# Kernel optimization log

Hardware: AMD Instinct MI355X
Metric: run time of the kernel (lower is better)

The kernel has to match this reference:

```python
import jax, jax.numpy as jnp
import numpy as np

# Dims: B batch, T snippets, DV visual feat (1024), DA audio feat (128),
# H hid_dim (128), DF ffn dim (512), KC classifier kernel (7)
B, T, DV, DA, H, DF, KC = 128, 256, 1024, 128, 128, 512, 7


def _xavier(key, shape, fan_in, fan_out):
    a = (6.0 / (fan_in + fan_out)) ** 0.5
    return jax.random.uniform(key, shape, jnp.float32, -a, a)


def setup_inputs() -> dict:
    key = jax.random.key(0)
    ks = jax.random.split(key, 9)
    return {
        "x": jax.random.normal(ks[0], (B, T, DV + DA), jnp.float32),
        # CrossAttention: q from audio (DA->H), k,v from visual (DV->H), out proj H->DV
        "Wq": _xavier(ks[1], (DA, H), DA, H), "bq": jnp.zeros((H,), jnp.float32),
        "Wk": _xavier(ks[2], (DV, H), DV, H), "bk": jnp.zeros((H,), jnp.float32),
        "Wv": _xavier(ks[3], (DV, H), DV, H), "bv": jnp.zeros((H,), jnp.float32),
        "Wo": _xavier(ks[4], (H, DV), H, DV), "bo": jnp.zeros((DV,), jnp.float32),
        # LayerNorm over modal_a=1024
        "ln_g": jnp.ones((DV,), jnp.float32), "ln_b": jnp.zeros((DV,), jnp.float32),
        # FFN: Conv1d(1024,512,1) -> GELU -> Conv1d(512,128,1) == two linears over channels
        "W1": _xavier(ks[5], (DV, DF), DV, DF), "b1": jnp.zeros((DF,), jnp.float32),
        "W2": _xavier(ks[6], (DF, H), DF, H), "b2": jnp.zeros((H,), jnp.float32),
        # Classifier: Conv1d(128, 1, kernel=7), OIH layout
        "Wc": _xavier(ks[7], (1, H, KC), H * KC, KC), "bc": jnp.zeros((1,), jnp.float32),
    }


def _distance_adj(t: int) -> jnp.ndarray:
    # adj[i, j] = exp(-|i - j| / e)  (DistanceAdj from the repo)
    idx = jnp.arange(t, dtype=jnp.float32)
    return jnp.exp(-jnp.abs(idx[:, None] - idx[None, :]) / jnp.float32(np.e))


def reference(x, Wq, bq, Wk, bk, Wv, bv, Wo, bo, ln_g, ln_b, W1, b1, W2, b2, Wc, bc):
    f_v = x[:, :, :DV]   # [B, T, 1024]
    f_a = x[:, :, DV:]   # [B, T, 128]
    adj = _distance_adj(T)  # [T, T], broadcast over batch

    # Cross attention: query from audio, key/value from visual, adjacency bias
    q = f_a @ Wq + bq                               # [B, T, H]
    k = f_v @ Wk + bk                               # [B, T, H]
    v = f_v @ Wv + bv                               # [B, T, H]
    scores = jnp.einsum('bqh,bkh->bqk', q, k) / jnp.sqrt(jnp.float32(H)) + adj
    attn = jax.nn.softmax(scores, axis=-1)
    ctx = jnp.einsum('bqk,bkh->bqh', attn, v)       # [B, T, H]
    ca_out = ctx @ Wo + bo                          # [B, T, 1024]

    # residual + LayerNorm(modal_a)
    h = f_v + ca_out
    mu = jnp.mean(h, axis=-1, keepdims=True)
    var = jnp.mean(jnp.square(h - mu), axis=-1, keepdims=True)
    h = (h - mu) * jax.lax.rsqrt(var + 1e-5) * ln_g + ln_b

    # conv1d(k=1) FFN: 1024 -> 512 -> GELU -> 128 (dropout = identity at eval)
    h = jax.nn.gelu(h @ W1 + b1, approximate=False) @ W2 + b2   # [B, T, 128]

    # causal left pad 6, then Conv1d(128 -> 1, kernel 7)
    hc = jnp.pad(jnp.transpose(h, (0, 2, 1)), ((0, 0), (0, 0), (KC - 1, 0)))  # [B, 128, T+6]
    logits = jax.lax.conv_general_dilated(
        hc, Wc, window_strides=(1,), padding='VALID',
        dimension_numbers=('NCH', 'OIH', 'NCH')) + bc[None, :, None]           # [B, 1, T]
    return jax.nn.sigmoid(logits[:, 0, :])                                      # [B, T]
```

## Files before the change

### kernel.cpp

```cpp
#include <hip/hip_runtime.h>
#include <hip/hip_bf16.h>
#include <math.h>

#define BB 128
#define TT 256
#define DV 1024
#define DA 128
#define HH 128
#define DF 512
#define KC 7
#define MM (BB*TT)

typedef __attribute__((ext_vector_type(8))) short    short8v;
typedef __attribute__((ext_vector_type(8))) _Float16 half8v;
typedef __attribute__((ext_vector_type(4))) float    float4v;

__device__ __forceinline__ float gelu_exact(float v) {
    return 0.5f * v * (1.0f + erff(v * 0.70710678118654752f));
}
__device__ __forceinline__ ushort f2h(float f) {
    _Float16 h = (_Float16)f;
    return __builtin_bit_cast(ushort, h);
}
__device__ __forceinline__ float h2f(ushort u) {
    _Float16 h = __builtin_bit_cast(_Float16, u);
    return (float)h;
}

__global__ __launch_bounds__(256) void wconv_kernel(const float* __restrict__ W,
                                                    ushort* __restrict__ Th,
                                                    int K, int N)
{
    __shared__ float sT[64][65];
    const int n0 = blockIdx.x * 64, k0 = blockIdx.y * 64;
    const int t = threadIdx.x;
    const int kk = t >> 4, n4 = (t & 15) * 4;
#pragma unroll
    for (int i = 0; i < 4; ++i) {
        float4 f = *(const float4*)(W + (size_t)(k0 + kk + i * 16) * N + n0 + n4);
        sT[kk + i * 16][n4 + 0] = f.x;
        sT[kk + i * 16][n4 + 1] = f.y;
        sT[kk + i * 16][n4 + 2] = f.z;
        sT[kk + i * 16][n4 + 3] = f.w;
    }
    __syncthreads();
    const int n = t >> 2, kq = (t & 3) * 16;
    ushort hh[16];
#pragma unroll
    for (int j = 0; j < 16; ++j) hh[j] = f2h(sT[kq + j][n]);
    ushort* dh = Th + (size_t)(n0 + n) * K + k0 + kq;
#pragma unroll
    for (int j = 0; j < 16; j += 4)
        *(ushort4*)(dh + j) = make_ushort4(hh[j], hh[j+1], hh[j+2], hh[j+3]);
}

__global__ __launch_bounds__(256) void bcat_kernel(const float* __restrict__ a,
                                                   const float* __restrict__ b,
                                                   float* __restrict__ dst)
{
    const int t = threadIdx.x;
    dst[t] = (t < 128) ? a[t] : b[t - 128];
}

template<int BM, int A_F32, int OUT>
__global__ __launch_bounds__(256) void mgemm(const void* __restrict__ Av, int lda,
                                             const ushort* __restrict__ Bt,
                                             const float* __restrict__ bias,
                                             void* __restrict__ Cv,
                                             int N, int K)
{
    constexpr int MF = BM / 32;
    __shared__ __align__(16) ushort smem[8192];
    auto Ah = (ushort (*)[BM][8])(smem);
    auto Bh = (ushort (*)[128][8])(smem + 4 * BM * 8);

    const int nwg = gridDim.x * gridDim.y;
    const int hid = blockIdx.y * gridDim.x + blockIdx.x;
    const int d   = (hid & 7) * (nwg >> 3) + (hid >> 3);
    const int bx  = d % gridDim.x, by = d / gridDim.x;

    const int tid = threadIdx.x;
    const int l = tid & 63;
    const int w = tid >> 6;
    const int wrow = (w >> 1) * (MF * 16), wcol = (w & 1) * 64;
    const int m0 = by * BM, n0 = bx * 128;

    float4v acc[MF][4];
#pragma unroll
    for (int m = 0; m < MF; ++m)
#pragma unroll
        for (int n = 0; n < 4; ++n) acc[m][n] = (float4v){0.f, 0.f, 0.f, 0.f};

    for (int k0 = 0; k0 < K; k0 += 32) {
        __syncthreads();
        if (A_F32) {
            if (BM == 128) {
                const int srow = tid >> 1, kh = (tid & 1) * 16;
                const float* Ap = (const float*)Av + (size_t)(m0 + srow) * lda + k0 + kh;
#pragma unroll
                for (int i = 0; i < 4; ++i) {
                    float4 f = *(const float4*)(Ap + i * 4);
                    *(ushort4*)&Ah[(kh >> 3) + (i >> 1)][srow][(i & 1) * 4] =
                        make_ushort4(f2h(f.x), f2h(f.y), f2h(f.z), f2h(f.w));
                }
            } else {
                const int srow = tid >> 2, ko = (tid & 3) * 8;
                const float* Ap = (const float*)Av + (size_t)(m0 + srow) * lda + k0 + ko;
#pragma unroll
                for (int i = 0; i < 2; ++i) {
                    float4 f = *(const float4*)(Ap + i * 4);
                    *(ushort4*)&Ah[ko >> 3][srow][i * 4] =
                        make_ushort4(f2h(f.x), f2h(f.y), f2h(f.z), f2h(f.w));
                }
            }
        } else {
            if (BM == 128) {
                const int srow = tid >> 1, kh = (tid & 1) * 16;
                const ushort* Ap = (const ushort*)Av + (size_t)(m0 + srow) * lda + k0 + kh;
                *(short8v*)&Ah[(kh >> 3) + 0][srow][0] = *(const short8v*)(Ap + 0);
                *(short8v*)&Ah[(kh >> 3) + 1][srow][0] = *(const short8v*)(Ap + 8);
            } else {
                const int srow = tid >> 2, ko = (tid & 3) * 8;
                const ushort* Ap = (const ushort*)Av + (size_t)(m0 + srow) * lda + k0 + ko;
                *(short8v*)&Ah[ko >> 3][srow][0] = *(const short8v*)Ap;
            }
        }
        {
            const int srow = tid >> 1, kh = (tid & 1) * 16;
            const ushort* Bp = Bt + (size_t)(n0 + srow) * K + k0 + kh;
            *(short8v*)&Bh[(kh >> 3) + 0][srow][0] = *(const short8v*)(Bp + 0);
            *(short8v*)&Bh[(kh >> 3) + 1][srow][0] = *(const short8v*)(Bp + 8);
        }
        __syncthreads();

        const int g = l >> 4, lr = l & 15;
        half8v af[MF], bf_[4];
#pragma unroll
        for (int m = 0; m < MF; ++m)
            af[m] = *(const half8v*)&Ah[g][wrow + m * 16 + lr][0];
#pragma unroll
        for (int n = 0; n < 4; ++n)
            bf_[n] = *(const half8v*)&Bh[g][wcol + n * 16 + lr][0];
#pragma unroll
        for (int m = 0; m < MF; ++m)
#pragma unroll
            for (int n = 0; n < 4; ++n)
                acc[m][n] = __builtin_amdgcn_mfma_f32_16x16x32_f16(af[m], bf_[n], acc[m][n], 0, 0, 0);
    }

    {
        const int g2 = l >> 4, lr = l & 15;
        constexpr int RPP = (OUT == 0) ? 32 : 64;
#pragma unroll
        for (int row0 = 0; row0 < BM; row0 += RPP) {
            __syncthreads();
#pragma unroll
            for (int m = 0; m < MF; ++m) {
                const int rbase = wrow + m * 16 + g2 * 4;
                if (rbase >= row0 && rbase < row0 + RPP) {
#pragma unroll
                    for (int n = 0; n < 4; ++n) {
                        const int col = wcol + n * 16 + lr;
                        const float bv = bias[n0 + col];
#pragma unroll
                        for (int r = 0; r < 4; ++r) {
                            const float o = acc[m][n][r] + bv;
                            const int lrow = rbase + r - row0;
                            if (OUT == 0)      ((float*)smem)[lrow * 128 + col] = o;
                            else if (OUT == 1) smem[lrow * 128 + col] = f2h(gelu_exact(o));
                            else               smem[lrow * 128 + col] = f2h(o);
                        }
                    }
                }
            }
            __syncthreads();
            if (OUT == 0) {
#pragma unroll
                for (int it = 0; it < (RPP * 128) / (4 * 256); ++it) {
                    const int u = tid + it * 256;
                    const int rr = u >> 5, cc = (u & 31) * 4;
                    *(float4*)&((float*)Cv)[(size_t)(m0 + row0 + rr) * N + n0 + cc] =
                        *(float4*)&((float*)smem)[rr * 128 + cc];
                }
            } else {
#pragma unroll
                for (int it = 0; it < (RPP * 128) / (8 * 256); ++it) {
                    const int u = tid + it * 256;
                    const int rr = u >> 4, cc = (u & 15) * 8;
                    *(short8v*)&((ushort*)Cv)[(size_t)(m0 + row0 + rr) * N + n0 + cc] =
                        *(short8v*)&smem[rr * 128 + cc];
                }
            }
        }
    }
}

__global__ __launch_bounds__(256) void scores_kernel(const float* __restrict__ q,
                                                     const float* __restrict__ kv,
                                                     float* __restrict__ S)
{
    const int kh = blockIdx.x;
    const int qh = blockIdx.y;
    const int b  = blockIdx.z;
    const int tid = threadIdx.x;
    const int tr = tid >> 4;
    const int tc = tid & 15;

    __shared__ float sA[32][68];
    __shared__ float sB[32][132];

    const float* Ab = q + ((size_t)b * TT + qh * 64) * HH;
    const float* Bb = kv + ((size_t)b * TT + kh * 128) * 256;

    float acc[4][8];
#pragma unroll
    for (int i = 0; i < 4; ++i)
#pragma unroll
        for (int j = 0; j < 8; ++j) acc[i][j] = 0.0f;

    for (int k0 = 0; k0 < 128; k0 += 32) {
        __syncthreads();
#pragma unroll
        for (int ll = 0; ll < 2; ++ll) {
            int f = tid + ll * 256;
            int row = f >> 3, c4 = f & 7;
            float4 val = *(const float4*)(Ab + (size_t)row * HH + k0 + c4 * 4);
            sA[c4 * 4 + 0][row] = val.x;
            sA[c4 * 4 + 1][row] = val.y;
            sA[c4 * 4 + 2][row] = val.z;
            sA[c4 * 4 + 3][row] = val.w;
        }
#pragma unroll
        for (int ll = 0; ll < 4; ++ll) {
            int f = tid + ll * 256;
            int row = f >> 3, c4 = f & 7;
            float4 val = *(const float4*)(Bb + (size_t)row * 256 + k0 + c4 * 4);
            sB[c4 * 4 + 0][row] = val.x;
            sB[c4 * 4 + 1][row] = val.y;
            sB[c4 * 4 + 2][row] = val.z;
            sB[c4 * 4 + 3][row] = val.w;
        }
        __syncthreads();
#pragma unroll
        for (int kk = 0; kk < 32; ++kk) {
            float4 a4 = *(const float4*)&sA[kk][tr * 4];
            float4 b0 = *(const float4*)&sB[kk][tc * 8];
            float4 b1 = *(const float4*)&sB[kk][tc * 8 + 4];
            float a[4]  = {a4.x, a4.y, a4.z, a4.w};
            float bb[8] = {b0.x, b0.y, b0.z, b0.w, b1.x, b1.y, b1.z, b1.w};
#pragma unroll
            for (int i = 0; i < 4; ++i)
#pragma unroll
                for (int j = 0; j < 8; ++j) acc[i][j] += a[i] * bb[j];
        }
    }

    const float scale = 0.088388347648318447f;
    const float inv_e = 0.36787944117144233f;
#pragma unroll
    for (int i = 0; i < 4; ++i) {
        int rq = qh * 64 + tr * 4 + i;
        float* srow = S + ((size_t)b * TT + rq) * TT + kh * 128 + tc * 8;
        float o[8];
#pragma unroll
        for (int j = 0; j < 8; ++j) {
            int ck = kh * 128 + tc * 8 + j;
            float adj = expf(-fabsf((float)(rq - ck)) * inv_e);
            o[j] = acc[i][j] * scale + adj;
        }
        *(float4*)srow       = make_float4(o[0], o[1], o[2], o[3]);
        *(float4*)(srow + 4) = make_float4(o[4], o[5], o[6], o[7]);
    }
}

__global__ __launch_bounds__(256) void softmax_kernel(float* __restrict__ S)
{
    const int row  = blockIdx.x * 4 + (threadIdx.x >> 6);
    const int lane = threadIdx.x & 63;
    float* p = S + (size_t)row * TT + lane * 4;
    float4 v = *(float4*)p;
    float m = fmaxf(fmaxf(v.x, v.y), fmaxf(v.z, v.w));
#pragma unroll
    for (int mask = 1; mask < 64; mask <<= 1) m = fmaxf(m, __shfl_xor(m, mask));
    float e0 = expf(v.x - m), e1 = expf(v.y - m), e2 = expf(v.z - m), e3 = expf(v.w - m);
    float s = e0 + e1 + e2 + e3;
#pragma unroll
    for (int mask = 1; mask < 64; mask <<= 1) s += __shfl_xor(s, mask);
    float inv = 1.0f / s;
    *(float4*)p = make_float4(e0 * inv, e1 * inv, e2 * inv, e3 * inv);
}

__global__ __launch_bounds__(256) void pv_kernel(const float* __restrict__ S,
                                                 const float* __restrict__ kv,
                                                 ushort* __restrict__ ctx)
{
    const int qh = blockIdx.x;
    const int b  = blockIdx.y;
    const int tid = threadIdx.x;
    const int tr = tid >> 4;
    const int tc = tid & 15;

    __shared__ float sA[32][68];
    __shared__ float sB[32][132];

    const float* Ab = S + ((size_t)b * TT + qh * 64) * TT;
    const float* Bb = kv + (size_t)b * TT * 256 + 128;

    float acc[4][8];
#pragma unroll
    for (int i = 0; i < 4; ++i)
#pragma unroll
        for (int j = 0; j < 8; ++j) acc[i][j] = 0.0f;

    for (int k0 = 0; k0 < 256; k0 += 32) {
        __syncthreads();
#pragma unroll
        for (int ll = 0; ll < 2; ++ll) {
            int f = tid + ll * 256;
            int row = f >> 3, c4 = f & 7;
            float4 val = *(const float4*)(Ab + (size_t)row * TT + k0 + c4 * 4);
            sA[c4 * 4 + 0][row] = val.x;
            sA[c4 * 4 + 1][row] = val.y;
            sA[c4 * 4 + 2][row] = val.z;
            sA[c4 * 4 + 3][row] = val.w;
        }
#pragma unroll
        for (int ll = 0; ll < 4; ++ll) {
            int f = tid + ll * 256;
            int row = f >> 5, c4 = f & 31;
            float4 val = *(const float4*)(Bb + (size_t)(k0 + row) * 256 + c4 * 4);
            *(float4*)&sB[row][c4 * 4] = val;
        }
        __syncthreads();
#pragma unroll
        for (int kk = 0; kk < 32; ++kk) {
            float4 a4 = *(const float4*)&sA[kk][tr * 4];
            float4 b0 = *(const float4*)&sB[kk][tc * 8];
            float4 b1 = *(const float4*)&sB[kk][tc * 8 + 4];
            float a[4]  = {a4.x, a4.y, a4.z, a4.w};
            float bb[8] = {b0.x, b0.y, b0.z, b0.w, b1.x, b1.y, b1.z, b1.w};
#pragma unroll
            for (int i = 0; i < 4; ++i)
#pragma unroll
                for (int j = 0; j < 8; ++j) acc[i][j] += a[i] * bb[j];
        }
    }

#pragma unroll
    for (int i = 0; i < 4; ++i) {
        ushort* crow = ctx + ((size_t)b * TT + qh * 64 + tr * 4 + i) * HH + tc * 8;
        *(ushort4*)crow       = make_ushort4(f2h(acc[i][0]), f2h(acc[i][1]),
                                             f2h(acc[i][2]), f2h(acc[i][3]));
        *(ushort4*)(crow + 4) = make_ushort4(f2h(acc[i][4]), f2h(acc[i][5]),
                                             f2h(acc[i][6]), f2h(acc[i][7]));
    }
}

__global__ __launch_bounds__(256) void resln_kernel(const float* __restrict__ x,
                                                    const ushort* __restrict__ ca16,
                                                    ushort* __restrict__ h16,
                                                    const float* __restrict__ gam,
                                                    const float* __restrict__ bet)
{
    const int row = blockIdx.x;
    const int tid = threadIdx.x;
    const float4 f = *(const float4*)(x + (size_t)row * 1152 + tid * 4);
    const ushort4 c4v = *(const ushort4*)(ca16 + (size_t)row * 1024 + tid * 4);
    float4 h;
    h.x = f.x + h2f(c4v.x); h.y = f.y + h2f(c4v.y);
    h.z = f.z + h2f(c4v.z); h.w = f.w + h2f(c4v.w);

    float s  = h.x + h.y + h.z + h.w;
    float ss = h.x * h.x + h.y * h.y + h.z * h.z + h.w * h.w;
#pragma unroll
    for (int m = 1; m < 64; m <<= 1) {
        s  += __shfl_xor(s, m);
        ss += __shfl_xor(ss, m);
    }
    __shared__ float red[8];
    if ((tid & 63) == 0) {
        red[tid >> 6]       = s;
        red[4 + (tid >> 6)] = ss;
    }
    __syncthreads();
    s  = red[0] + red[1] + red[2] + red[3];
    ss = red[4] + red[5] + red[6] + red[7];
    const float mean = s * (1.0f / 1024.0f);
    const float var  = ss * (1.0f / 1024.0f) - mean * mean;
    const float rstd = 1.0f / sqrtf(var + 1e-5f);

    const float4 g4 = *(const float4*)(gam + tid * 4);
    const float4 b4 = *(const float4*)(bet + tid * 4);
    ushort* hout = h16 + (size_t)row * 1024 + tid * 4;
    *(ushort4*)hout = make_ushort4(
        f2h((h.x - mean) * rstd * g4.x + b4.x),
        f2h((h.y - mean) * rstd * g4.y + b4.y),
        f2h((h.z - mean) * rstd * g4.z + b4.z),
        f2h((h.w - mean) * rstd * g4.w + b4.w));
}

__global__ __launch_bounds__(256) void conv_kernel(const float* __restrict__ h2,
                                                   const float* __restrict__ Wc,
                                                   const float* __restrict__ bcp,
                                                   float* __restrict__ out)
{
    const int t0 = blockIdx.x * 64;
    const int b  = blockIdx.y;
    const int tid = threadIdx.x;

    __shared__ float sw[896];
    __shared__ float sh[70][130];
    __shared__ float red[4][64];

    for (int i = tid; i < 896; i += 256) sw[i] = Wc[i];
    for (int f = tid; f < 70 * 32; f += 256) {
        int rr = f >> 5, c4 = f & 31;
        int trow = t0 - 6 + rr;
        float4 val = make_float4(0.f, 0.f, 0.f, 0.f);
        if (trow >= 0)
            val = *(const float4*)(h2 + ((size_t)b * TT + trow) * HH + c4 * 4);
        sh[rr][c4 * 4 + 0] = val.x;
        sh[rr][c4 * 4 + 1] = val.y;
        sh[rr][c4 * 4 + 2] = val.z;
        sh[rr][c4 * 4 + 3] = val.w;
    }
    __syncthreads();

    const int tt  = tid & 63;
    const int grp = tid >> 6;
    const int i0  = grp * 32;
    float acc = 0.0f;
    for (int j = 0; j < 7; ++j) {
        const int srow2 = tt + j;
#pragma unroll
        for (int i2 = 0; i2 < 16; ++i2) {
            float2 hv = *(const float2*)&sh[srow2][i0 + i2 * 2];
            acc += hv.x * sw[(i0 + i2 * 2) * 7 + j] + hv.y * sw[(i0 + i2 * 2 + 1) * 7 + j];
        }
    }
    red[grp][tt] = acc;
    __syncthreads();
    if (grp == 0) {
        float tot = red[0][tt] + red[1][tt] + red[2][tt] + red[3][tt] + bcp[0];
        out[(size_t)b * TT + t0 + tt] = 1.0f / (1.0f + expf(-tot));
    }
}

extern "C" void kernel_launch(void* const* d_in, const int* in_sizes, int n_in,
                              void* d_out, int out_size, void* d_ws, size_t ws_size,
                              hipStream_t stream)
{
    const float* x   = (const float*)d_in[0];
    const float* Wq  = (const float*)d_in[1];
    const float* bq  = (const float*)d_in[2];
    const float* Wk  = (const float*)d_in[3];
    const float* bk  = (const float*)d_in[4];
    const float* Wv  = (const float*)d_in[5];
    const float* bv  = (const float*)d_in[6];
    const float* Wo  = (const float*)d_in[7];
    const float* bo  = (const float*)d_in[8];
    const float* lng = (const float*)d_in[9];
    const float* lnb = (const float*)d_in[10];
    const float* W1  = (const float*)d_in[11];
    const float* b1  = (const float*)d_in[12];
    const float* W2  = (const float*)d_in[13];
    const float* b2  = (const float*)d_in[14];
    const float* Wc  = (const float*)d_in[15];
    const float* bc  = (const float*)d_in[16];
    float* out = (float*)d_out;
    char* wsb = (char*)d_ws;

    ushort* WT   = (ushort*)wsb;
    const size_t oWq  = 0;
    const size_t oWkv = 16384;
    const size_t oWo  = 278528;
    const size_t oW1  = 409600;
    const size_t oW2  = 933888;
    float*  bkv  = (float*)(wsb + 2097152);
    float*  qb   = (float*)(wsb + 4194304);
    float*  kvb  = (float*)(wsb + 20971520);
    ushort* ctxb = (ushort*)(wsb + 54525952);
    float*  Sbuf = (float*)(wsb + 62914560);
    ushort* ca16 = (ushort*)(wsb + 62914560);
    ushort* h16  = (ushort*)(wsb + 130023424);
    ushort* hf   = (ushort*)(wsb + 4194304);
    float*  h2   = (float*)(wsb + 37748736);

    dim3 thr(256);
    wconv_kernel<<<dim3(2, 2),  thr, 0, stream>>>(Wq, WT + oWq, 128, 128);
    wconv_kernel<<<dim3(2, 16), thr, 0, stream>>>(Wk, WT + oWkv, 1024, 128);
    wconv_kernel<<<dim3(2, 16), thr, 0, stream>>>(Wv, WT + oWkv + 128 * 1024, 1024, 128);
    wconv_kernel<<<dim3(16, 2), thr, 0, stream>>>(Wo, WT + oWo, 128, 1024);
    wconv_kernel<<<dim3(8, 16), thr, 0, stream>>>(W1, WT + oW1, 1024, 512);
    wconv_kernel<<<dim3(2, 8),  thr, 0, stream>>>(W2, WT + oW2, 512, 128);
    bcat_kernel<<<dim3(1), thr, 0, stream>>>(bk, bv, bkv);

    mgemm<64, 1, 0><<<dim3(2, 512), thr, 0, stream>>>(x,        1152, WT + oWkv, bkv, kvb, 256, 1024);
    mgemm<64, 1, 0><<<dim3(1, 512), thr, 0, stream>>>(x + 1024, 1152, WT + oWq,  bq,  qb,  128, 128);
    scores_kernel <<<dim3(2, 4, 128), thr, 0, stream>>>(qb, kvb, Sbuf);
    softmax_kernel<<<dim3(MM / 4),    thr, 0, stream>>>(Sbuf);
    pv_kernel     <<<dim3(4, 128),    thr, 0, stream>>>(Sbuf, kvb, ctxb);
    mgemm<128, 0, 2><<<dim3(8, 256), thr, 0, stream>>>(ctxb, 128, WT + oWo, bo, ca16, 1024, 128);
    resln_kernel<<<dim3(MM), thr, 0, stream>>>(x, ca16, h16, lng, lnb);
    mgemm<128, 0, 1><<<dim3(4, 256), thr, 0, stream>>>(h16, 1024, WT + oW1, b1, hf, 512, 1024);
    mgemm<64, 0, 0><<<dim3(1, 512), thr, 0, stream>>>(hf, 512, WT + oW2, b2, h2, 128, 512);
    conv_kernel<<<dim3(4, 128), thr, 0, stream>>>(h2, Wc, bc, out);
}
```

Baseline: 588.0 us.

## Pre-convert input to fp16 and stage GEMM tiles with direct global-to-LDS loads

Adds a pass that converts the whole fp32 input x to fp16 in workspace, so every GEMM takes fp16 A operands. The GEMM tile loads now use global_load_lds (16-byte direct-to-LDS transfers) with precomputed per-wave addresses, replacing register-staged loads and in-loop fp32-to-fp16 conversion. This is meant to cut VGPR traffic and instruction count in the GEMM main loop. The price is an extra full read and write of x (about 150 MB fp32 read plus 75 MB fp16 write) and a different LDS fill pattern.

```diff
diff --git a/kernel.cpp b/kernel.cpp
--- a/kernel.cpp
+++ b/kernel.cpp
@@ -26,6 +26,22 @@
     _Float16 h = __builtin_bit_cast(_Float16, u);
     return (float)h;
 }
+__device__ __forceinline__ void gload16(const ushort* g, const ushort* l) {
+    __builtin_amdgcn_global_load_lds(
+        (const __attribute__((address_space(1))) unsigned int*)g,
+        (__attribute__((address_space(3))) unsigned int*)l,
+        16, 0, 0);
+}
+
+__global__ __launch_bounds__(256) void xconv_kernel(const float* __restrict__ x,
+                                                    ushort* __restrict__ o)
+{
+    const size_t u = ((size_t)blockIdx.x * 256 + threadIdx.x) * 8;
+    float4 a = *(const float4*)(x + u);
+    float4 b = *(const float4*)(x + u + 4);
+    *(ushort4*)(o + u)     = make_ushort4(f2h(a.x), f2h(a.y), f2h(a.z), f2h(a.w));
+    *(ushort4*)(o + u + 4) = make_ushort4(f2h(b.x), f2h(b.y), f2h(b.z), f2h(b.w));
+}
 
 __global__ __launch_bounds__(256) void wconv_kernel(const float* __restrict__ W,
                                                     ushort* __restrict__ Th,
@@ -62,8 +78,8 @@
     dst[t] = (t < 128) ? a[t] : b[t - 128];
 }
 
-template<int BM, int A_F32, int OUT>
-__global__ __launch_bounds__(256) void mgemm(const void* __restrict__ Av, int lda,
+template<int BM, int OUT>
+__global__ __launch_bounds__(256) void mgemm(const ushort* __restrict__ Aq, int lda,
                                              const ushort* __restrict__ Bt,
                                              const float* __restrict__ bias,
                                              void* __restrict__ Cv,
@@ -91,46 +107,34 @@
 #pragma unroll
         for (int n = 0; n < 4; ++n) acc[m][n] = (float4v){0.f, 0.f, 0.f, 0.f};
 
+    constexpr int NA  = BM / 16;
+    constexpr int NCH = (NA + 8) / 4;
+    const ushort* gs[NCH];
+    const ushort* ls[NCH];
+    {
+        int ci = 0;
+#pragma unroll
+        for (int c = w; c < NA + 8; c += 4, ++ci) {
+            if (c < NA) {
+                const int kg = c / (BM / 64);
+                const int r0 = (c % (BM / 64)) * 64;
+                gs[ci] = Aq + (size_t)(m0 + r0 + l) * lda + kg * 8;
+                ls[ci] = smem + (kg * BM + r0) * 8;
+            } else {
+                const int bc = c - NA;
+                const int kg = bc >> 1;
+                const int r0 = (bc & 1) * 64;
+                gs[ci] = Bt + (size_t)(n0 + r0 + l) * K + kg * 8;
+                ls[ci] = smem + 4 * BM * 8 + (kg * 128 + r0) * 8;
+            }
+        }
+    }
+
     for (int k0 = 0; k0 < K; k0 += 32) {
         __syncthreads();
-        if (A_F32) {
-            if (BM == 128) {
-                const int srow = tid >> 1, kh = (tid & 1) * 16;
-                const float* Ap = (const float*)Av + (size_t)(m0 + srow) * lda + k0 + kh;
-#pragma unroll
-                for (int i = 0; i < 4; ++i) {
-                    float4 f = *(const float4*)(Ap + i * 4);
-                    *(ushort4*)&Ah[(kh >> 3) + (i >> 1)][srow][(i & 1) * 4] =
-                        make_ushort4(f2h(f.x), f2h(f.y), f2h(f.z), f2h(f.w));
-                }
-            } else {
-                const int srow = tid >> 2, ko = (tid & 3) * 8;
-                const float* Ap = (const float*)Av + (size_t)(m0 + srow) * lda + k0 + ko;
-#pragma unroll
-                for (int i = 0; i < 2; ++i) {
-                    float4 f = *(const float4*)(Ap + i * 4);
-                    *(ushort4*)&Ah[ko >> 3][srow][i * 4] =
-                        make_ushort4(f2h(f.x), f2h(f.y), f2h(f.z), f2h(f.w));
-                }
-            }
-        } else {
-            if (BM == 128) {
-                const int srow = tid >> 1, kh = (tid & 1) * 16;
-                const ushort* Ap = (const ushort*)Av + (size_t)(m0 + srow) * lda + k0 + kh;
-                *(short8v*)&Ah[(kh >> 3) + 0][srow][0] = *(const short8v*)(Ap + 0);
-                *(short8v*)&Ah[(kh >> 3) + 1][srow][0] = *(const short8v*)(Ap + 8);
-            } else {
-                const int srow = tid >> 2, ko = (tid & 3) * 8;
-                const ushort* Ap = (const ushort*)Av + (size_t)(m0 + srow) * lda + k0 + ko;
-                *(short8v*)&Ah[ko >> 3][srow][0] = *(const short8v*)Ap;
-            }
-        }
-        {
-            const int srow = tid >> 1, kh = (tid & 1) * 16;
-            const ushort* Bp = Bt + (size_t)(n0 + srow) * K + k0 + kh;
-            *(short8v*)&Bh[(kh >> 3) + 0][srow][0] = *(const short8v*)(Bp + 0);
-            *(short8v*)&Bh[(kh >> 3) + 1][srow][0] = *(const short8v*)(Bp + 8);
-        }
+#pragma unroll
+        for (int i = 0; i < NCH; ++i)
+            gload16(gs[i] + k0, ls[i]);
         __syncthreads();
 
         const int g = l >> 4, lr = l & 15;
@@ -481,6 +485,7 @@
     float*  kvb  = (float*)(wsb + 20971520);
     ushort* ctxb = (ushort*)(wsb + 54525952);
     float*  Sbuf = (float*)(wsb + 62914560);
+    ushort* x16  = (ushort*)(wsb + 96468992);
     ushort* ca16 = (ushort*)(wsb + 62914560);
     ushort* h16  = (ushort*)(wsb + 130023424);
     ushort* hf   = (ushort*)(wsb + 4194304);
@@ -494,15 +499,16 @@
     wconv_kernel<<<dim3(8, 16), thr, 0, stream>>>(W1, WT + oW1, 1024, 512);
     wconv_kernel<<<dim3(2, 8),  thr, 0, stream>>>(W2, WT + oW2, 512, 128);
     bcat_kernel<<<dim3(1), thr, 0, stream>>>(bk, bv, bkv);
-
-    mgemm<64, 1, 0><<<dim3(2, 512), thr, 0, stream>>>(x,        1152, WT + oWkv, bkv, kvb, 256, 1024);
-    mgemm<64, 1, 0><<<dim3(1, 512), thr, 0, stream>>>(x + 1024, 1152, WT + oWq,  bq,  qb,  128, 128);
+    xconv_kernel<<<dim3(MM * 1152 / (256 * 8)), thr, 0, stream>>>(x, x16);
+
+    mgemm<64, 0><<<dim3(2, 512), thr, 0, stream>>>(x16,        1152, WT + oWkv, bkv, kvb, 256, 1024);
+    mgemm<64, 0><<<dim3(1, 512), thr, 0, stream>>>(x16 + 1024, 1152, WT + oWq,  bq,  qb,  128, 128);
     scores_kernel <<<dim3(2, 4, 128), thr, 0, stream>>>(qb, kvb, Sbuf);
     softmax_kernel<<<dim3(MM / 4),    thr, 0, stream>>>(Sbuf);
     pv_kernel     <<<dim3(4, 128),    thr, 0, stream>>>(Sbuf, kvb, ctxb);
-    mgemm<128, 0, 2><<<dim3(8, 256), thr, 0, stream>>>(ctxb, 128, WT + oWo, bo, ca16, 1024, 128);
+    mgemm<128, 2><<<dim3(8, 256), thr, 0, stream>>>(ctxb, 128, WT + oWo, bo, ca16, 1024, 128);
     resln_kernel<<<dim3(MM), thr, 0, stream>>>(x, ca16, h16, lng, lnb);
-    mgemm<128, 0, 1><<<dim3(4, 256), thr, 0, stream>>>(h16, 1024, WT + oW1, b1, hf, 512, 1024);
-    mgemm<64, 0, 0><<<dim3(1, 512), thr, 0, stream>>>(hf, 512, WT + oW2, b2, h2, 128, 512);
+    mgemm<128, 1><<<dim3(4, 256), thr, 0, stream>>>(h16, 1024, WT + oW1, b1, hf, 512, 1024);
+    mgemm<64, 0><<<dim3(1, 512), thr, 0, stream>>>(hf, 512, WT + oW2, b2, h2, 128, 512);
     conv_kernel<<<dim3(4, 128), thr, 0, stream>>>(h2, Wc, bc, out);
 }
```

Result: slower. 642.6 us (+9.3%).
